# Performance work log

Hardware: AMD Instinct MI355X
Metric: run time of the kernel (lower is better)

Reference implementation:

```python
import jax, jax.numpy as jnp
import numpy as np
import math

GAMMA = 0.97      # discounting
LAM = 0.95        # gae lambda
EPSILON = 0.3     # ppo clip
EPS = 0.2         # gpo clip (eps)
ENT_COST = 0.01
RSCALE = 1.0
ALPHA = 1.0
NUM_STEPS = 1.0e6 # normalization step count buffer


def _mlp(x, Ws, bs):
    for i, (W, b) in enumerate(zip(Ws, bs)):
        x = x @ W.T + b
        if i < len(Ws) - 1:
            x = jax.nn.silu(x)
    return x


def _dist_create(logits):
    loc, s = jnp.split(logits, 2, axis=-1)
    return loc, jax.nn.softplus(s) + 0.001


def _log_det_jac(x):
    # tanh bijector log|det J| per element
    return 2.0 * (math.log(2.0) - x - jax.nn.softplus(-2.0 * x))


def _log_prob(loc, scale, dist):
    lu = -0.5 * jnp.square((dist - loc) / scale)
    ln = 0.5 * math.log(2.0 * math.pi) + jnp.log(scale)
    return (lu - ln - _log_det_jac(dist)).sum(-1)


def _entropy(loc, scale, noise):
    ln = 0.5 * math.log(2.0 * math.pi) + jnp.log(scale)
    ent = (0.5 + ln) * jnp.ones_like(loc)
    dist = loc + scale * noise  # reparameterized sample (torch.normal)
    return (ent + _log_det_jac(dist)).sum(-1)


def _kl(pl, ps, ql, qs):
    vr = jnp.square(ps / qs)
    t1 = jnp.square((pl - ql) / qs)
    return (0.5 * (vr + t1 - 1.0 - jnp.log(vr))).mean(-1)


def _normalize(obs, rm, rv):
    var = jnp.clip(rv / (NUM_STEPS + 1.0), 1e-6, 1e6)
    return jnp.clip((obs - rm) / jnp.sqrt(var), -5.0, 5.0)


def _gae(truncation, termination, reward, values, bootstrap_value):
    tm = 1.0 - truncation
    v1 = jnp.concatenate([values[1:], bootstrap_value[None]], 0)
    deltas = (reward + GAMMA * (1.0 - termination) * v1 - values) * tm

    def step(acc, xs):
        d, te, tmask = xs
        acc = d + GAMMA * (1.0 - te) * tmask * LAM * acc
        return acc, acc

    _, vmx = jax.lax.scan(step, jnp.zeros_like(bootstrap_value),
                          (deltas, termination, tm), reverse=True)
    vs = vmx + values
    vs1 = jnp.concatenate([vs[1:], bootstrap_value[None]], 0)
    adv = (reward + GAMMA * (1.0 - termination) * vs1 - values) * tm
    return vs, adv


def _loss(observation, pobservation, reward, done, truncation, logits, action,
          noise, pw0, pb0, pw1, pb1, pw2, pb2, vw0, vb0, vw1, vb1, vw2, vb2,
          running_mean, running_variance, kl_coef):
    sg = jax.lax.stop_gradient
    Pw, Pb = [pw0, pw1, pw2], [pb0, pb1, pb2]
    Vw, Vb = [vw0, vw1, vw2], [vb0, vb1, vb2]

    obs_n = _normalize(observation, running_mean, running_variance)
    pobs_n = _normalize(pobservation, running_mean, running_variance)

    guider_logits = _mlp(obs_n[:-1], Pw, Pb)
    learner_logits = _mlp(pobs_n[:-1], Pw, Pb)
    baseline = _mlp(obs_n, Vw, Vb).squeeze(-1)  # [T+1, B]
    bootstrap = baseline[-1]
    baseline = baseline[:-1]

    reward_s = reward * RSCALE
    termination = done * (1.0 - truncation)

    loc, scale = _dist_create(logits)
    b_lp = _log_prob(loc, scale, action)
    gl, gs = _dist_create(guider_logits)
    g_lp = _log_prob(gl, gs, action)
    ll, ls = _dist_create(learner_logits)
    l_lp = _log_prob(ll, ls, action)

    kl_learner = _kl(sg(gl), sg(gs), ll, ls).mean()
    kl_guider = _kl(gl, gs, sg(ll), sg(ls))
    # use_clip = True branch
    diff = g_lp - l_lp
    m = jnp.where(diff > math.log(1.0 + EPS), 1.0,
                  jnp.where(diff < math.log(1.0 - EPS), 1.0, 0.0))
    kl_guider = (kl_guider * m).mean()

    vs, adv = _gae(truncation, termination, reward_s, sg(baseline), sg(bootstrap))
    vs = sg(vs)
    adv = sg((adv - adv.mean()) / (jnp.std(adv, ddof=1) + 1e-5))

    rho = jnp.exp(g_lp - b_lp)
    rho_clip = jnp.exp(jnp.clip(g_lp - sg(l_lp), math.log(1.0 - EPS), math.log(1.0 + EPS))
                       + sg(l_lp) - b_lp)
    rho_clip = jnp.clip(rho_clip, 1.0 - EPSILON, 1.0 + EPSILON)
    guider_policy_loss = -jnp.mean(jnp.minimum(rho * adv, rho_clip * adv))

    rho2 = jnp.exp(jnp.minimum(l_lp - b_lp, 10.0))  # stable_exp
    rho2c = jnp.clip(rho2, 1.0 - EPSILON, 1.0 + EPSILON)
    learner_policy_loss = -jnp.mean(jnp.minimum(rho2 * adv, rho2c * adv))

    v_err = vs - baseline
    v_loss = jnp.mean(v_err * v_err) * 0.25

    entropy = jnp.mean(_entropy(loc, scale, noise))
    entropy_loss = -ENT_COST * entropy

    learner_loss = kl_learner + learner_policy_loss * ALPHA  # use_clip
    guider_loss = kl_guider + guider_policy_loss
    total = learner_loss + guider_loss + v_loss + entropy_loss
    return total, guider_loss, learner_loss, kl_learner


def setup_inputs() -> dict:
    key = jax.random.key(0)
    T, B, OBS, ACT, H = 1024, 256, 64, 8, 256
    ks = iter(jax.random.split(key, 32))

    def lin(fin, fout):
        W = jax.random.normal(next(ks), (fout, fin), jnp.float32) / np.float32(np.sqrt(fin))
        b = jnp.zeros((fout,), jnp.float32)
        return W, b

    pw0, pb0 = lin(OBS, H); pw1, pb1 = lin(H, H); pw2, pb2 = lin(H, 2 * ACT)
    vw0, vb0 = lin(OBS, H); vw1, vb1 = lin(H, H); vw2, vb2 = lin(H, 1)

    observation = jax.random.normal(next(ks), (T + 1, B, OBS), jnp.float32)
    pobservation = observation + 0.1 * jax.random.normal(next(ks), (T + 1, B, OBS), jnp.float32)
    reward = jax.random.normal(next(ks), (T, B), jnp.float32)
    done = (jax.random.uniform(next(ks), (T, B)) < 0.01).astype(jnp.float32)
    truncation = (jax.random.uniform(next(ks), (T, B)) < 0.005).astype(jnp.float32)
    logits = 0.5 * jax.random.normal(next(ks), (T, B, 2 * ACT), jnp.float32)
    action = jax.random.normal(next(ks), (T, B, ACT), jnp.float32)
    noise = jax.random.normal(next(ks), (T, B, ACT), jnp.float32)
    running_mean = jnp.zeros((OBS,), jnp.float32)
    running_variance = jnp.ones((OBS,), jnp.float32) * NUM_STEPS  # unit variance after /num_steps
    kl_coef = jnp.ones((1,), jnp.float32)

    return {"observation": observation, "pobservation": pobservation,
            "reward": reward, "done": done, "truncation": truncation,
            "logits": logits, "action": action, "noise": noise,
            "pw0": pw0, "pb0": pb0, "pw1": pw1, "pb1": pb1, "pw2": pw2, "pb2": pb2,
            "vw0": vw0, "vb0": vb0, "vw1": vw1, "vb1": vb1, "vw2": vw2, "vb2": vb2,
            "running_mean": running_mean, "running_variance": running_variance,
            "kl_coef": kl_coef}


def reference(observation, pobservation, reward, done, truncation, logits, action,
              noise, pw0, pb0, pw1, pb1, pw2, pb2, vw0, vb0, vw1, vb1, vw2, vb2,
              running_mean, running_variance, kl_coef):
    return _loss(observation, pobservation, reward, done, truncation, logits,
                 action, noise, pw0, pb0, pw1, pb1, pw2, pb2, vw0, vb0, vw1, vb1,
                 vw2, vb2, running_mean, running_variance, kl_coef)
```

## Files before the change

### kernel.cpp

```cpp
#include <hip/hip_runtime.h>
#include <math.h>

#define GAMMA_   0.97f
#define LAM_     0.95f
#define EPSILON_ 0.3f
#define HLOG2PI_ 0.91893853320467274f
#define LOG2C_   0.69314718055994531f
#define LOG1P2_  0.18232155679395463f
#define LOG0P8_  (-0.22314355131420976f)

typedef unsigned short u16;
typedef unsigned int   u32;
typedef _Float16 half8 __attribute__((ext_vector_type(8)));
typedef _Float16 half4 __attribute__((ext_vector_type(4)));
typedef __attribute__((ext_vector_type(4))) float floatx4;
typedef __attribute__((ext_vector_type(8))) float floatx8;

constexpr int  TT     = 1024;
constexpr long ROWS_P = (long)TT * 256;
constexpr long ROWS_V = (long)(TT + 1) * 256;

constexpr long FR_W0P_HI = 0;
constexpr long FR_W0P_LO = 16384;
constexpr long FR_W1P_HI = 32768;
constexpr long FR_W1P_LO = 98304;
constexpr long FR_W2P_HI = 163840;
constexpr long FR_W2P_LO = 167936;
constexpr long FR_W0V_HI = 172032;
constexpr long FR_W0V_LO = 188416;
constexpr long FR_W1V_HI = 204800;
constexpr long FR_W1V_LO = 270336;
constexpr long FR_W2V_HI = 335872;
constexpr long FR_W2V_LO = 339968;
constexpr long FR_TOTAL  = 344064;

constexpr long WS_ACC  = 0;
constexpr long WS_INV  = 32;
constexpr long WS_ADV  = 96;
constexpr long WS_BASE = WS_ADV + ROWS_P;
constexpr long WS_GA   = WS_BASE + ROWS_V;
constexpr long WS_GP   = WS_GA + 8192;
constexpr long WS_BANK = WS_GP + 8192;
constexpr long WS_GLP  = WS_BANK + 1024;
constexpr long WS_LLP  = WS_GLP + ROWS_P;
constexpr long WS_BLP  = WS_LLP + ROWS_P;


__device__ __forceinline__ float softplus_f(float x) {
  return (x > 20.f) ? x : log1pf(expf(x));
}
__device__ __forceinline__ float silu_f(float x) {
  return x * __builtin_amdgcn_rcpf(1.f + __expf(-x));
}
__device__ __forceinline__ float clamp30(float x) {
  return fminf(1e30f, fmaxf(-1e30f, x));
}

__global__ void convert_kernel(const float* __restrict__ pw0,
                               const float* __restrict__ pw1,
                               const float* __restrict__ pw2,
                               const float* __restrict__ vw0,
                               const float* __restrict__ vw1,
                               const float* __restrict__ vw2,
                               const float* __restrict__ rv,
                               float* __restrict__ inv_std,
                               float* __restrict__ accum,
                               float* __restrict__ accumB,
                               u16* __restrict__ frag) {
  if (blockIdx.x == 0) {
    int t = threadIdx.x;
    if (t < 32) accum[t] = 0.f;
    for (int i = t; i < 1024; i += 256) accumB[i] = 0.f;
    if (t < 64) {
      float var = rv[t] / 1000001.0f;
      var = fminf(1e6f, fmaxf(1e-6f, var));
      inv_std[t] = 1.f / sqrtf(var);
    }
  }
  int idx = blockIdx.x * 256 + threadIdx.x;
  const float* W; int kslog, K, nvalid; long hioff, looff; int e;
  if (idx < 16384)       { W = pw0; e = idx;          kslog = 1; K = 64;  nvalid = 256; hioff = FR_W0P_HI; looff = FR_W0P_LO; }
  else if (idx < 81920)  { W = pw1; e = idx - 16384;  kslog = 3; K = 256; nvalid = 256; hioff = FR_W1P_HI; looff = FR_W1P_LO; }
  else if (idx < 86016)  { W = pw2; e = idx - 81920;  kslog = 3; K = 256; nvalid = 16;  hioff = FR_W2P_HI; looff = FR_W2P_LO; }
  else if (idx < 102400) { W = vw0; e = idx - 86016;  kslog = 1; K = 64;  nvalid = 256; hioff = FR_W0V_HI; looff = FR_W0V_LO; }
  else if (idx < 167936) { W = vw1; e = idx - 102400; kslog = 3; K = 256; nvalid = 256; hioff = FR_W1V_HI; looff = FR_W1V_LO; }
  else                   { W = vw2; e = idx - 167936; kslog = 3; K = 256; nvalid = 1;   hioff = FR_W2V_HI; looff = FR_W2V_LO; }
  int j    = e & 7;
  int lane = (e >> 3) & 63;
  int ks   = (e >> 9) & ((1 << kslog) - 1);
  int nt   = e >> (9 + kslog);
  int n = nt * 16 + (lane & 15);
  int k = ks * 32 + ((lane >> 4) << 3) + j;
  float w = (n < nvalid) ? W[n * K + k] : 0.f;
  _Float16 hi = (_Float16)w;
  _Float16 lo = (_Float16)(w - (float)hi);
  frag[hioff + e] = *(u16*)&hi;
  frag[looff + e] = *(u16*)&lo;
}

constexpr int SX = 72;
constexpr int SH = 264;
constexpr int SO = 20;

__global__ __launch_bounds__(256, 3)
void fused_fwd_kernel(const float* __restrict__ obs,
                      const float* __restrict__ pobs,
                      const float* __restrict__ rm,
                      const float* __restrict__ inv_std,
                      const u16* __restrict__ frag,
                      const float* __restrict__ pb0,
                      const float* __restrict__ pb1,
                      const float* __restrict__ pb2,
                      const float* __restrict__ vb0,
                      const float* __restrict__ vb1,
                      const float* __restrict__ vb2,
                      const float* __restrict__ logits,
                      const float* __restrict__ action,
                      const float* __restrict__ noise,
                      float* __restrict__ baseline,
                      float* __restrict__ glpA,
                      float* __restrict__ llpA,
                      float* __restrict__ blpA,
                      float* __restrict__ accumB) {
  __shared__ __align__(16) _Float16 H[64 * SH];
  __shared__ __align__(16) float OUTT[64 * SO];
  __shared__ float red[192];

  const int tid  = threadIdx.x;
  const int lane = tid & 63;
  const int wv   = tid >> 6;
  const int lm   = lane & 15;
  const int lq   = lane >> 4;

  int bid = blockIdx.x;
  bool isP; long sub;
  if (bid < 12288) {
    int g = bid / 3, r = bid - g * 3;
    if (r < 2) { isP = true;  sub = (long)g * 2 + r; }
    else       { isP = false; sub = g; }
  } else { isP = false; sub = 4096 + (bid - 12288); }

  _Float16* X = H;

  if (isP) {
    const long row0 = sub * 32;
    #pragma unroll
    for (int it = 0; it < 2; ++it) {
      int flat = it * 256 + tid;
      int vr = flat >> 3;
      int f0 = (flat & 7) * 8;
      const float* src = (vr < 32) ? obs : pobs;
      floatx8 v  = *(const floatx8*)&src[(row0 + (vr & 31)) * 64 + f0];
      floatx8 m  = *(const floatx8*)&rm[f0];
      floatx8 is = *(const floatx8*)&inv_std[f0];
      half8 h;
      #pragma unroll
      for (int j = 0; j < 8; ++j)
        h[j] = (_Float16)fminf(5.f, fmaxf(-5.f, (v[j] - m[j]) * is[j]));
      *(half8*)&X[vr * SX + f0] = h;
    }

    const int  er   = tid >> 3;
    const int  ed   = tid & 7;
    const long erow = row0 + er;
    float pf_a   = action[erow * 8 + ed];
    float pf_loc = logits[erow * 16 + ed];
    float pf_sr  = logits[erow * 16 + 8 + ed];
    float pf_nd  = noise[erow * 8 + ed];

    const half8* B0h = (const half8*)(frag + FR_W0P_HI);
    const half8* B0l = (const half8*)(frag + FR_W0P_LO);
    half8 B0hr[2][4], B0lr[2][4];
    #pragma unroll
    for (int ks = 0; ks < 2; ++ks)
      #pragma unroll
      for (int nt = 0; nt < 4; ++nt) {
        int ntg = wv * 4 + nt;
        B0hr[ks][nt] = B0h[(ntg * 2 + ks) * 64 + lane];
        B0lr[ks][nt] = B0l[(ntg * 2 + ks) * 64 + lane];
      }

    floatx4 acc[4][4];
    #pragma unroll
    for (int nt = 0; nt < 4; ++nt) {
      floatx4 bz = *(const floatx4*)&pb0[(wv * 4 + nt) * 16 + lq * 4];
      #pragma unroll
      for (int mt = 0; mt < 4; ++mt) acc[mt][nt] = bz;
    }
    __syncthreads();

    #pragma unroll
    for (int ks = 0; ks < 2; ++ks) {
      half8 A[4];
      #pragma unroll
      for (int mt = 0; mt < 4; ++mt)
        A[mt] = *(const half8*)&X[(mt * 16 + lm) * SX + ks * 32 + lq * 8];
      __builtin_amdgcn_s_setprio(1);
      #pragma unroll
      for (int mt = 0; mt < 4; ++mt)
        #pragma unroll
        for (int nt = 0; nt < 4; ++nt)
          acc[mt][nt] = __builtin_amdgcn_mfma_f32_16x16x32_f16(B0hr[ks][nt], A[mt], acc[mt][nt], 0, 0, 0);
      #pragma unroll
      for (int mt = 0; mt < 4; ++mt)
        #pragma unroll
        for (int nt = 0; nt < 4; ++nt)
          acc[mt][nt] = __builtin_amdgcn_mfma_f32_16x16x32_f16(B0lr[ks][nt], A[mt], acc[mt][nt], 0, 0, 0);
      __builtin_amdgcn_s_setprio(0);
    }

    const half8* B1h = (const half8*)(frag + FR_W1P_HI);
    const half8* B1l = (const half8*)(frag + FR_W1P_LO);
    half8 Bh[4], Bl[4], Bhn[4], Bln[4];
    #pragma unroll
    for (int nt = 0; nt < 4; ++nt) {
      int ntg = wv * 4 + nt;
      Bh[nt] = B1h[(ntg * 8) * 64 + lane];
      Bl[nt] = B1l[(ntg * 8) * 64 + lane];
    }

    __syncthreads();
    #pragma unroll
    for (int nt = 0; nt < 4; ++nt) {
      int colbase = (wv * 4 + nt) * 16 + lq * 4;
      #pragma unroll
      for (int mt = 0; mt < 4; ++mt) {
        int row = mt * 16 + lm;
        half4 h;
        #pragma unroll
        for (int reg = 0; reg < 4; ++reg)
          h[reg] = (_Float16)silu_f(acc[mt][nt][reg]);
        *(half4*)&H[row * SH + colbase] = h;
      }
    }
    #pragma unroll
    for (int nt = 0; nt < 4; ++nt) {
      floatx4 bz = *(const floatx4*)&pb1[(wv * 4 + nt) * 16 + lq * 4];
      #pragma unroll
      for (int mt = 0; mt < 4; ++mt) acc[mt][nt] = bz;
    }
    __syncthreads();

    #pragma unroll 1
    for (int ks = 0; ks < 8; ++ks) {
      if (ks < 7) {
        #pragma unroll
        for (int nt = 0; nt < 4; ++nt) {
          int ntg = wv * 4 + nt;
          Bhn[nt] = B1h[(ntg * 8 + ks + 1) * 64 + lane];
          Bln[nt] = B1l[(ntg * 8 + ks + 1) * 64 + lane];
        }
      }
      half8 A[4];
      #pragma unroll
      for (int mt = 0; mt < 4; ++mt)
        A[mt] = *(const half8*)&H[(mt * 16 + lm) * SH + ks * 32 + lq * 8];
      __builtin_amdgcn_s_setprio(1);
      #pragma unroll
      for (int mt = 0; mt < 4; ++mt)
        #pragma unroll
        for (int nt = 0; nt < 4; ++nt)
          acc[mt][nt] = __builtin_amdgcn_mfma_f32_16x16x32_f16(Bh[nt], A[mt], acc[mt][nt], 0, 0, 0);
      #pragma unroll
      for (int mt = 0; mt < 4; ++mt)
        #pragma unroll
        for (int nt = 0; nt < 4; ++nt)
          acc[mt][nt] = __builtin_amdgcn_mfma_f32_16x16x32_f16(Bl[nt], A[mt], acc[mt][nt], 0, 0, 0);
      __builtin_amdgcn_s_setprio(0);
      if (ks < 7) {
        #pragma unroll
        for (int nt = 0; nt < 4; ++nt) { Bh[nt] = Bhn[nt]; Bl[nt] = Bln[nt]; }
      }
    }

    const half8* B2h = (const half8*)(frag + FR_W2P_HI);
    const half8* B2l = (const half8*)(frag + FR_W2P_LO);
    half8 B2hr[8], B2lr[8];
    #pragma unroll
    for (int ks = 0; ks < 8; ++ks) {
      B2hr[ks] = B2h[ks * 64 + lane];
      B2lr[ks] = B2l[ks * 64 + lane];
    }

    __syncthreads();
    #pragma unroll
    for (int nt = 0; nt < 4; ++nt) {
      int colbase = (wv * 4 + nt) * 16 + lq * 4;
      #pragma unroll
      for (int mt = 0; mt < 4; ++mt) {
        int row = mt * 16 + lm;
        half4 h;
        #pragma unroll
        for (int reg = 0; reg < 4; ++reg)
          h[reg] = (_Float16)silu_f(acc[mt][nt][reg]);
        *(half4*)&H[row * SH + colbase] = h;
      }
    }
    __syncthreads();

    {
      floatx4 c3a = (floatx4){0.f,0.f,0.f,0.f};
      floatx4 c3b = (floatx4){0.f,0.f,0.f,0.f};
      __builtin_amdgcn_s_setprio(1);
      #pragma unroll
      for (int ks = 0; ks < 8; ks += 2) {
        half8 A0 = *(const half8*)&H[(wv * 16 + lm) * SH + ks * 32 + lq * 8];
        half8 A1 = *(const half8*)&H[(wv * 16 + lm) * SH + (ks + 1) * 32 + lq * 8];
        c3a = __builtin_amdgcn_mfma_f32_16x16x32_f16(B2hr[ks],     A0, c3a, 0, 0, 0);
        c3b = __builtin_amdgcn_mfma_f32_16x16x32_f16(B2hr[ks + 1], A1, c3b, 0, 0, 0);
        c3a = __builtin_amdgcn_mfma_f32_16x16x32_f16(B2lr[ks],     A0, c3a, 0, 0, 0);
        c3b = __builtin_amdgcn_mfma_f32_16x16x32_f16(B2lr[ks + 1], A1, c3b, 0, 0, 0);
      }
      __builtin_amdgcn_s_setprio(0);
      floatx4 bias = *(const floatx4*)&pb2[lq * 4];
      floatx4 o = c3a + c3b + bias;
      #pragma unroll
      for (int reg = 0; reg < 4; ++reg)
        OUTT[(wv * 16 + lm) * SO + lq * 4 + reg] = o[reg];
    }
    __syncthreads();

    {
      int r = er, d = ed;
      float gl  = OUTT[r * SO + d];
      float gsr = OUTT[r * SO + 8 + d];
      float ll  = OUTT[(32 + r) * SO + d];
      float lsr = OUTT[(32 + r) * SO + 8 + d];
      float a   = pf_a;
      float loc = pf_loc;
      float sr  = pf_sr;
      float nd  = pf_nd;

      float gs = softplus_f(gsr) + 1e-3f;
      float ls = softplus_f(lsr) + 1e-3f;
      float sc = softplus_f(sr) + 1e-3f;
      float ldj = 2.f * (LOG2C_ - a - softplus_f(-2.f * a));
      float lgs = logf(gs), lls = logf(ls), lsc = logf(sc);
      float zg = (a - gl) / gs;
      float zl = (a - ll) / ls;
      float z  = (a - loc) / sc;
      float glp = -0.5f * zg * zg - lgs - HLOG2PI_ - ldj;
      float llp = -0.5f * zl * zl - lls - HLOG2PI_ - ldj;
      float blp = -0.5f * z * z - lsc - HLOG2PI_ - ldj;
      float ratio = gs / ls;
      float vr = ratio * ratio;
      float t1 = (gl - ll) / ls; t1 *= t1;
      float kl = 0.5f * (vr + t1 - 1.f) - (lgs - lls);
      float dist = loc + sc * nd;
      float ent = 0.5f + HLOG2PI_ + lsc
                + 2.f * (LOG2C_ - dist - softplus_f(-2.f * dist));

      #pragma unroll
      for (int o = 4; o > 0; o >>= 1) {
        glp += __shfl_down(glp, o, 8);
        llp += __shfl_down(llp, o, 8);
        blp += __shfl_down(blp, o, 8);
        kl  += __shfl_down(kl, o, 8);
        ent += __shfl_down(ent, o, 8);
      }

      if (d == 0) {
        kl *= 0.125f;
        kl  = clamp30(kl);
        ent = clamp30(ent);
        float diff = glp - llp;
        float m = (diff > LOG1P2_ || diff < LOG0P8_) ? 1.f : 0.f;
        red[r]        = kl;
        red[32 + r]   = kl * m;
        red[64 + r]   = ent;
        red[96 + r]   = glp;
        red[128 + r]  = llp;
        red[160 + r]  = blp;
      }
    }
    __syncthreads();
    if (tid < 96) {
      int a = tid >> 5, i = tid & 31;
      float v = red[96 + tid];
      float* dst = (a == 0) ? glpA : (a == 1) ? llpA : blpA;
      dst[row0 + i] = v;
    }
    if (tid < 32) {
      float s0 = red[tid], s1 = red[32 + tid], s2 = red[64 + tid];
      #pragma unroll
      for (int o = 16; o > 0; o >>= 1) {
        s0 += __shfl_down(s0, o, 32);
        s1 += __shfl_down(s1, o, 32);
        s2 += __shfl_down(s2, o, 32);
      }
      if (tid == 0) {
        float* bank = accumB + (bid & 31) * 32;
        atomicAdd(&bank[0], s0);
        atomicAdd(&bank[1], s1);
        atomicAdd(&bank[2], s2);
      }
    }
  } else {
    const long row0 = sub * 64;
    #pragma unroll
    for (int it = 0; it < 2; ++it) {
      int flat = it * 256 + tid;
      int vr = flat >> 3;
      int f0 = (flat & 7) * 8;
      floatx8 v  = *(const floatx8*)&obs[(row0 + vr) * 64 + f0];
      floatx8 m  = *(const floatx8*)&rm[f0];
      floatx8 is = *(const floatx8*)&inv_std[f0];
      half8 h;
      #pragma unroll
      for (int j = 0; j < 8; ++j)
        h[j] = (_Float16)fminf(5.f, fmaxf(-5.f, (v[j] - m[j]) * is[j]));
      *(half8*)&X[vr * SX + f0] = h;
    }

    const half8* B0h = (const half8*)(frag + FR_W0V_HI);
    const half8* B0l = (const half8*)(frag + FR_W0V_LO);
    half8 B0hr[2][4], B0lr[2][4];
    #pragma unroll
    for (int ks = 0; ks < 2; ++ks)
      #pragma unroll
      for (int nt = 0; nt < 4; ++nt) {
        int ntg = wv * 4 + nt;
        B0hr[ks][nt] = B0h[(ntg * 2 + ks) * 64 + lane];
        B0lr[ks][nt] = B0l[(ntg * 2 + ks) * 64 + lane];
      }

    floatx4 acc[4][4];
    #pragma unroll
    for (int nt = 0; nt < 4; ++nt) {
      floatx4 bz = *(const floatx4*)&vb0[(wv * 4 + nt) * 16 + lq * 4];
      #pragma unroll
      for (int mt = 0; mt < 4; ++mt) acc[mt][nt] = bz;
    }
    __syncthreads();

    #pragma unroll
    for (int ks = 0; ks < 2; ++ks) {
      half8 A[4];
      #pragma unroll
      for (int mt = 0; mt < 4; ++mt)
        A[mt] = *(const half8*)&X[(mt * 16 + lm) * SX + ks * 32 + lq * 8];
      __builtin_amdgcn_s_setprio(1);
      #pragma unroll
      for (int mt = 0; mt < 4; ++mt)
        #pragma unroll
        for (int nt = 0; nt < 4; ++nt)
          acc[mt][nt] = __builtin_amdgcn_mfma_f32_16x16x32_f16(B0hr[ks][nt], A[mt], acc[mt][nt], 0, 0, 0);
      #pragma unroll
      for (int mt = 0; mt < 4; ++mt)
        #pragma unroll
        for (int nt = 0; nt < 4; ++nt)
          acc[mt][nt] = __builtin_amdgcn_mfma_f32_16x16x32_f16(B0lr[ks][nt], A[mt], acc[mt][nt], 0, 0, 0);
      __builtin_amdgcn_s_setprio(0);
    }

    const half8* B1h = (const half8*)(frag + FR_W1V_HI);
    const half8* B1l = (const half8*)(frag + FR_W1V_LO);
    half8 Bh[4], Bl[4], Bhn[4], Bln[4];
    #pragma unroll
    for (int nt = 0; nt < 4; ++nt) {
      int ntg = wv * 4 + nt;
      Bh[nt] = B1h[(ntg * 8) * 64 + lane];
      Bl[nt] = B1l[(ntg * 8) * 64 + lane];
    }

    __syncthreads();
    #pragma unroll
    for (int nt = 0; nt < 4; ++nt) {
      int colbase = (wv * 4 + nt) * 16 + lq * 4;
      #pragma unroll
      for (int mt = 0; mt < 4; ++mt) {
        int row = mt * 16 + lm;
        half4 h;
        #pragma unroll
        for (int reg = 0; reg < 4; ++reg)
          h[reg] = (_Float16)silu_f(acc[mt][nt][reg]);
        *(half4*)&H[row * SH + colbase] = h;
      }
    }
    #pragma unroll
    for (int nt = 0; nt < 4; ++nt) {
      floatx4 bz = *(const floatx4*)&vb1[(wv * 4 + nt) * 16 + lq * 4];
      #pragma unroll
      for (int mt = 0; mt < 4; ++mt) acc[mt][nt] = bz;
    }
    __syncthreads();

    #pragma unroll 1
    for (int ks = 0; ks < 8; ++ks) {
      if (ks < 7) {
        #pragma unroll
        for (int nt = 0; nt < 4; ++nt) {
          int ntg = wv * 4 + nt;
          Bhn[nt] = B1h[(ntg * 8 + ks + 1) * 64 + lane];
          Bln[nt] = B1l[(ntg * 8 + ks + 1) * 64 + lane];
        }
      }
      half8 A[4];
      #pragma unroll
      for (int mt = 0; mt < 4; ++mt)
        A[mt] = *(const half8*)&H[(mt * 16 + lm) * SH + ks * 32 + lq * 8];
      __builtin_amdgcn_s_setprio(1);
      #pragma unroll
      for (int mt = 0; mt < 4; ++mt)
        #pragma unroll
        for (int nt = 0; nt < 4; ++nt)
          acc[mt][nt] = __builtin_amdgcn_mfma_f32_16x16x32_f16(Bh[nt], A[mt], acc[mt][nt], 0, 0, 0);
      #pragma unroll
      for (int mt = 0; mt < 4; ++mt)
        #pragma unroll
        for (int nt = 0; nt < 4; ++nt)
          acc[mt][nt] = __builtin_amdgcn_mfma_f32_16x16x32_f16(Bl[nt], A[mt], acc[mt][nt], 0, 0, 0);
      __builtin_amdgcn_s_setprio(0);
      if (ks < 7) {
        #pragma unroll
        for (int nt = 0; nt < 4; ++nt) { Bh[nt] = Bhn[nt]; Bl[nt] = Bln[nt]; }
      }
    }

    const half8* B2h = (const half8*)(frag + FR_W2V_HI);
    const half8* B2l = (const half8*)(frag + FR_W2V_LO);
    half8 B2hr[8], B2lr[8];
    #pragma unroll
    for (int ks = 0; ks < 8; ++ks) {
      B2hr[ks] = B2h[ks * 64 + lane];
      B2lr[ks] = B2l[ks * 64 + lane];
    }

    __syncthreads();
    #pragma unroll
    for (int nt = 0; nt < 4; ++nt) {
      int colbase = (wv * 4 + nt) * 16 + lq * 4;
      #pragma unroll
      for (int mt = 0; mt < 4; ++mt) {
        int row = mt * 16 + lm;
        half4 h;
        #pragma unroll
        for (int reg = 0; reg < 4; ++reg)
          h[reg] = (_Float16)silu_f(acc[mt][nt][reg]);
        *(half4*)&H[row * SH + colbase] = h;
      }
    }
    __syncthreads();

    {
      floatx4 c3a = (floatx4){0.f,0.f,0.f,0.f};
      floatx4 c3b = (floatx4){0.f,0.f,0.f,0.f};
      __builtin_amdgcn_s_setprio(1);
      #pragma unroll
      for (int ks = 0; ks < 8; ks += 2) {
        half8 A0 = *(const half8*)&H[(wv * 16 + lm) * SH + ks * 32 + lq * 8];
        half8 A1 = *(const half8*)&H[(wv * 16 + lm) * SH + (ks + 1) * 32 + lq * 8];
        c3a = __builtin_amdgcn_mfma_f32_16x16x32_f16(B2hr[ks],     A0, c3a, 0, 0, 0);
        c3b = __builtin_amdgcn_mfma_f32_16x16x32_f16(B2hr[ks + 1], A1, c3b, 0, 0, 0);
        c3a = __builtin_amdgcn_mfma_f32_16x16x32_f16(B2lr[ks],     A0, c3a, 0, 0, 0);
        c3b = __builtin_amdgcn_mfma_f32_16x16x32_f16(B2lr[ks + 1], A1, c3b, 0, 0, 0);
      }
      __builtin_amdgcn_s_setprio(0);
      if (lq == 0) baseline[row0 + wv * 16 + lm] = c3a[0] + c3b[0] + vb2[0];
    }
  }
}

__global__ void gae_phase1(const float* __restrict__ reward,
                           const float* __restrict__ done,
                           const float* __restrict__ trunc,
                           const float* __restrict__ baseline,
                           float* __restrict__ A, float* __restrict__ P) {
  int s = blockIdx.x, b = threadIdx.x;
  float Aa = 0.f, Pp = 1.f;
  for (int t = (s + 1) * 32 - 1; t >= s * 32; --t) {
    int idx = t * 256 + b;
    float r = reward[idx], d = done[idx], tr = trunc[idx];
    float tm = 1.f - tr;
    float te = d * tm;
    float bl = baseline[idx], bl1 = baseline[idx + 256];
    float g1 = GAMMA_ * (1.f - te);
    float delta = (r + g1 * bl1 - bl) * tm;
    float c = g1 * tm * LAM_;
    Aa = delta + c * Aa;
    Pp = c * Pp;
  }
  A[s * 256 + b] = Aa;
  P[s * 256 + b] = Pp;
}

__global__ void gae_phase3(const float* __restrict__ reward,
                           const float* __restrict__ done,
                           const float* __restrict__ trunc,
                           const float* __restrict__ baseline,
                           const float* __restrict__ A,
                           const float* __restrict__ P,
                           float* __restrict__ adv,
                           float* __restrict__ accum) {
  __shared__ float red[12];
  int s = blockIdx.x, b = threadIdx.x;
  float acc = 0.f;
  #pragma unroll 1
  for (int s2 = 31; s2 > s; --s2)
    acc = A[s2 * 256 + b] + P[s2 * 256 + b] * acc;
  int tend = (s + 1) * 32;
  float vnext = baseline[tend * 256 + b];
  float vs_next = acc + vnext;
  float sa = 0.f, sa2 = 0.f, sv2 = 0.f;
  for (int t = tend - 1; t >= s * 32; --t) {
    int idx = t * 256 + b;
    float r = reward[idx], d = done[idx], tr = trunc[idx];
    float tm = 1.f - tr;
    float te = d * tm;
    float bl = baseline[idx];
    float g1 = GAMMA_ * (1.f - te);
    float delta = (r + g1 * vnext - bl) * tm;
    acc = delta + g1 * tm * LAM_ * acc;
    float at = (r + g1 * vs_next - bl) * tm;
    at = fminf(1e15f, fmaxf(-1e15f, at));
    adv[idx] = at;
    sa += at; sa2 += at * at;
    sv2 += fminf(acc * acc, 1e30f);
    vs_next = acc + bl;
    vnext = bl;
  }
  float v0 = sa, v1 = sa2, v2 = sv2;
  #pragma unroll
  for (int o = 32; o > 0; o >>= 1) {
    v0 += __shfl_down(v0, o, 64);
    v1 += __shfl_down(v1, o, 64);
    v2 += __shfl_down(v2, o, 64);
  }
  int lane = threadIdx.x & 63, w = threadIdx.x >> 6;
  if (lane == 0) { red[w] = v0; red[4 + w] = v1; red[8 + w] = v2; }
  __syncthreads();
  if (threadIdx.x == 0) {
    float s0=0.f, s1=0.f, s2=0.f;
    for (int q = 0; q < 4; ++q) { s0 += red[q]; s1 += red[4+q]; s2 += red[8+q]; }
    atomicAdd(&accum[3], s0);
    atomicAdd(&accum[4], s1);
    atomicAdd(&accum[5], s2);
  }
}

__global__ __launch_bounds__(256)
void epi2_kernel(const float* __restrict__ glpA,
                 const float* __restrict__ llpA,
                 const float* __restrict__ blpA,
                 const float* __restrict__ adv,
                 float* __restrict__ accum,
                 float* __restrict__ accumB,
                 float* __restrict__ out) {
  __shared__ float red2[8];
  __shared__ int lastFlag;
  int tid = threadIdx.x;
  long row = (long)blockIdx.x * 256 + tid;

  float glp = glpA[row], llp = llpA[row], blp = blpA[row], av = adv[row];
  float N = (float)ROWS_P;
  float sum = accum[3], sumsq = accum[4];
  float mean = sum / N;
  float var  = fmaxf((sumsq - sum * sum / N) / (N - 1.f), 0.f);
  float inv  = 1.f / (sqrtf(var) + 1e-5f);
  float a_n  = (av - mean) * inv;

  float diff = glp - llp;
  float rho = expf(fminf(glp - blp, 80.f));
  float cl  = fminf(LOG1P2_, fmaxf(LOG0P8_, diff));
  float rc  = expf(fminf(cl + llp - blp, 80.f));
  rc = fminf(1.f + EPSILON_, fmaxf(1.f - EPSILON_, rc));
  float gp = clamp30(fminf(rho * a_n, rc * a_n));

  float rho2 = expf(fminf(llp - blp, 10.f));
  float r2c  = fminf(1.f + EPSILON_, fmaxf(1.f - EPSILON_, rho2));
  float lp = clamp30(fminf(rho2 * a_n, r2c * a_n));

  #pragma unroll
  for (int o = 32; o > 0; o >>= 1) {
    gp += __shfl_down(gp, o, 64);
    lp += __shfl_down(lp, o, 64);
  }
  int lane = tid & 63, w = tid >> 6;
  if (lane == 0) { red2[w] = gp; red2[4 + w] = lp; }
  __syncthreads();
  if (tid == 0) {
    float sg = 0.f, sl = 0.f;
    for (int q = 0; q < 4; ++q) { sg += red2[q]; sl += red2[4 + q]; }
    float* bank = accumB + (blockIdx.x & 31) * 32;
    atomicAdd(&bank[6], sg);
    atomicAdd(&bank[7], sl);
    __threadfence();
    u32 old = atomicAdd((u32*)&accum[24], 1u);
    lastFlag = (old == (u32)(gridDim.x - 1)) ? 1 : 0;
  }
  __syncthreads();
  if (lastFlag) {
    float s0 = 0.f, s1 = 0.f, s2 = 0.f, s6 = 0.f, s7 = 0.f;
    if (tid < 32) {
      float* bank = accumB + tid * 32;
      s0 = atomicAdd(&bank[0], 0.f);
      s1 = atomicAdd(&bank[1], 0.f);
      s2 = atomicAdd(&bank[2], 0.f);
      s6 = atomicAdd(&bank[6], 0.f);
      s7 = atomicAdd(&bank[7], 0.f);
    }
    #pragma unroll
    for (int o = 16; o > 0; o >>= 1) {
      s0 += __shfl_down(s0, o, 32);
      s1 += __shfl_down(s1, o, 32);
      s2 += __shfl_down(s2, o, 32);
      s6 += __shfl_down(s6, o, 32);
      s7 += __shfl_down(s7, o, 32);
    }
    if (tid == 0) {
      float kl_learner = s0 / N;
      float kl_guider  = s1 / N;
      float entropy    = s2 / N;
      float v_loss     = 0.25f * accum[5] / N;
      float gp_loss    = -s6 / N;
      float lp_loss    = -s7 / N;
      float learner_loss = kl_learner + lp_loss;
      float guider_loss  = kl_guider + gp_loss;
      float total = learner_loss + guider_loss + v_loss - 0.01f * entropy;
      out[0] = total;
      out[1] = guider_loss;
      out[2] = learner_loss;
      out[3] = kl_learner;
    }
  }
}

extern "C" void kernel_launch(void* const* d_in, const int* in_sizes, int n_in,
                              void* d_out, int out_size, void* d_ws, size_t ws_size,
                              hipStream_t stream) {
  (void)in_sizes; (void)n_in; (void)out_size; (void)ws_size;
  const float* obs    = (const float*)d_in[0];
  const float* pobs   = (const float*)d_in[1];
  const float* reward = (const float*)d_in[2];
  const float* done   = (const float*)d_in[3];
  const float* trunc  = (const float*)d_in[4];
  const float* logits = (const float*)d_in[5];
  const float* action = (const float*)d_in[6];
  const float* noise  = (const float*)d_in[7];
  const float* pw0 = (const float*)d_in[8];
  const float* pb0 = (const float*)d_in[9];
  const float* pw1 = (const float*)d_in[10];
  const float* pb1 = (const float*)d_in[11];
  const float* pw2 = (const float*)d_in[12];
  const float* pb2 = (const float*)d_in[13];
  const float* vw0 = (const float*)d_in[14];
  const float* vb0 = (const float*)d_in[15];
  const float* vw1 = (const float*)d_in[16];
  const float* vb1 = (const float*)d_in[17];
  const float* vw2 = (const float*)d_in[18];
  const float* vb2 = (const float*)d_in[19];
  const float* rm  = (const float*)d_in[20];
  const float* rv  = (const float*)d_in[21];

  u16*   frag  = (u16*)d_ws;
  float* fbase = (float*)d_ws + FR_TOTAL / 2;
  float* accum   = fbase + WS_ACC;
  float* inv_std = fbase + WS_INV;
  float* adv     = fbase + WS_ADV;
  float* base    = fbase + WS_BASE;
  float* gA      = fbase + WS_GA;
  float* gP      = fbase + WS_GP;
  float* accumB  = fbase + WS_BANK;
  float* glpA    = fbase + WS_GLP;
  float* llpA    = fbase + WS_LLP;
  float* blpA    = fbase + WS_BLP;
  float* out = (float*)d_out;

  convert_kernel<<<672, 256, 0, stream>>>(pw0, pw1, pw2, vw0, vw1, vw2,
                                          rv, inv_std, accum, accumB, frag);

  fused_fwd_kernel<<<12292, 256, 0, stream>>>(
      obs, pobs, rm, inv_std, frag, pb0, pb1, pb2, vb0, vb1, vb2,
      logits, action, noise, base, glpA, llpA, blpA, accumB);

  gae_phase1<<<32, 256, 0, stream>>>(reward, done, trunc, base, gA, gP);
  gae_phase3<<<32, 256, 0, stream>>>(reward, done, trunc, base, gA, gP,
                                     adv, accum);

  epi2_kernel<<<1024, 256, 0, stream>>>(glpA, llpA, blpA, adv,
                                        accum, accumB, out);
}
```

Before: 523.9 us.

## Merge GAE phases and epilogue into one cooperative kernel with grid syncs

Replaces three separate kernel launches (GAE phase 1, GAE phase 3 and the loss epilogue) with a single cooperative kernel of 256 blocks that uses grid.sync between stages. The epilogue now has each block handle four rows per thread, and the last-block atomic counter is replaced by a final grid sync after which block 0 reduces the banks. This aims to remove launch gaps and the ticket-based completion logic. In exchange the GAE stages run on only 32 of the 256 blocks while the rest wait at the barriers, and the kernel depends on cooperative launch support and co-residency of all blocks.

After: 598.4 us. 14.2% more time.

```diff
diff --git a/kernel.cpp b/kernel.cpp
--- a/kernel.cpp
+++ b/kernel.cpp
@@ -1,5 +1,8 @@
 #include <hip/hip_runtime.h>
+#include <hip/hip_cooperative_groups.h>
 #include <math.h>
+
+namespace cg = cooperative_groups;
 
 #define GAMMA_   0.97f
 #define LAM_     0.95f
@@ -561,143 +564,140 @@
   }
 }
 
-__global__ void gae_phase1(const float* __restrict__ reward,
-                           const float* __restrict__ done,
-                           const float* __restrict__ trunc,
-                           const float* __restrict__ baseline,
-                           float* __restrict__ A, float* __restrict__ P) {
-  int s = blockIdx.x, b = threadIdx.x;
-  float Aa = 0.f, Pp = 1.f;
-  for (int t = (s + 1) * 32 - 1; t >= s * 32; --t) {
-    int idx = t * 256 + b;
-    float r = reward[idx], d = done[idx], tr = trunc[idx];
-    float tm = 1.f - tr;
-    float te = d * tm;
-    float bl = baseline[idx], bl1 = baseline[idx + 256];
-    float g1 = GAMMA_ * (1.f - te);
-    float delta = (r + g1 * bl1 - bl) * tm;
-    float c = g1 * tm * LAM_;
-    Aa = delta + c * Aa;
-    Pp = c * Pp;
+__global__ __launch_bounds__(256)
+void gae_epi_kernel(const float* __restrict__ reward,
+                    const float* __restrict__ done,
+                    const float* __restrict__ trunc,
+                    const float* __restrict__ baseline,
+                    float* __restrict__ A, float* __restrict__ P,
+                    float* __restrict__ adv,
+                    const float* __restrict__ glpA,
+                    const float* __restrict__ llpA,
+                    const float* __restrict__ blpA,
+                    float* __restrict__ accum,
+                    float* __restrict__ accumB,
+                    float* __restrict__ out) {
+  cg::grid_group grid = cg::this_grid();
+  __shared__ float red[12];
+  __shared__ float red2[8];
+  const int tid = threadIdx.x;
+  const int bid = blockIdx.x;
+
+  if (bid < 32) {
+    int s = bid, b = tid;
+    float Aa = 0.f, Pp = 1.f;
+    for (int t = (s + 1) * 32 - 1; t >= s * 32; --t) {
+      int idx = t * 256 + b;
+      float r = reward[idx], d = done[idx], tr = trunc[idx];
+      float tm = 1.f - tr;
+      float te = d * tm;
+      float bl = baseline[idx], bl1 = baseline[idx + 256];
+      float g1 = GAMMA_ * (1.f - te);
+      float delta = (r + g1 * bl1 - bl) * tm;
+      float c = g1 * tm * LAM_;
+      Aa = delta + c * Aa;
+      Pp = c * Pp;
+    }
+    A[s * 256 + b] = Aa;
+    P[s * 256 + b] = Pp;
   }
-  A[s * 256 + b] = Aa;
-  P[s * 256 + b] = Pp;
-}
-
-__global__ void gae_phase3(const float* __restrict__ reward,
-                           const float* __restrict__ done,
-                           const float* __restrict__ trunc,
-                           const float* __restrict__ baseline,
-                           const float* __restrict__ A,
-                           const float* __restrict__ P,
-                           float* __restrict__ adv,
-                           float* __restrict__ accum) {
-  __shared__ float red[12];
-  int s = blockIdx.x, b = threadIdx.x;
-  float acc = 0.f;
-  #pragma unroll 1
-  for (int s2 = 31; s2 > s; --s2)
-    acc = A[s2 * 256 + b] + P[s2 * 256 + b] * acc;
-  int tend = (s + 1) * 32;
-  float vnext = baseline[tend * 256 + b];
-  float vs_next = acc + vnext;
-  float sa = 0.f, sa2 = 0.f, sv2 = 0.f;
-  for (int t = tend - 1; t >= s * 32; --t) {
-    int idx = t * 256 + b;
-    float r = reward[idx], d = done[idx], tr = trunc[idx];
-    float tm = 1.f - tr;
-    float te = d * tm;
-    float bl = baseline[idx];
-    float g1 = GAMMA_ * (1.f - te);
-    float delta = (r + g1 * vnext - bl) * tm;
-    acc = delta + g1 * tm * LAM_ * acc;
-    float at = (r + g1 * vs_next - bl) * tm;
-    at = fminf(1e15f, fmaxf(-1e15f, at));
-    adv[idx] = at;
-    sa += at; sa2 += at * at;
-    sv2 += fminf(acc * acc, 1e30f);
-    vs_next = acc + bl;
-    vnext = bl;
+  grid.sync();
+
+  if (bid < 32) {
+    int s = bid, b = tid;
+    float acc = 0.f;
+    #pragma unroll 1
+    for (int s2 = 31; s2 > s; --s2)
+      acc = A[s2 * 256 + b] + P[s2 * 256 + b] * acc;
+    int tend = (s + 1) * 32;
+    float vnext = baseline[tend * 256 + b];
+    float vs_next = acc + vnext;
+    float sa = 0.f, sa2 = 0.f, sv2 = 0.f;
+    for (int t = tend - 1; t >= s * 32; --t) {
+      int idx = t * 256 + b;
+      float r = reward[idx], d = done[idx], tr = trunc[idx];
+      float tm = 1.f - tr;
+      float te = d * tm;
+      float bl = baseline[idx];
+      float g1 = GAMMA_ * (1.f - te);
+      float delta = (r + g1 * vnext - bl) * tm;
+      acc = delta + g1 * tm * LAM_ * acc;
+      float at = (r + g1 * vs_next - bl) * tm;
+      at = fminf(1e15f, fmaxf(-1e15f, at));
+      adv[idx] = at;
+      sa += at; sa2 += at * at;
+      sv2 += fminf(acc * acc, 1e30f);
+      vs_next = acc + bl;
+      vnext = bl;
+    }
+    float v0 = sa, v1 = sa2, v2 = sv2;
+    #pragma unroll
+    for (int o = 32; o > 0; o >>= 1) {
+      v0 += __shfl_down(v0, o, 64);
+      v1 += __shfl_down(v1, o, 64);
+      v2 += __shfl_down(v2, o, 64);
+    }
+    int lane = tid & 63, w = tid >> 6;
+    if (lane == 0) { red[w] = v0; red[4 + w] = v1; red[8 + w] = v2; }
+    __syncthreads();
+    if (tid == 0) {
+      float s0 = 0.f, s1 = 0.f, s2 = 0.f;
+      for (int q = 0; q < 4; ++q) { s0 += red[q]; s1 += red[4+q]; s2 += red[8+q]; }
+      atomicAdd(&accum[3], s0);
+      atomicAdd(&accum[4], s1);
+      atomicAdd(&accum[5], s2);
+    }
   }
-  float v0 = sa, v1 = sa2, v2 = sv2;
-  #pragma unroll
-  for (int o = 32; o > 0; o >>= 1) {
-    v0 += __shfl_down(v0, o, 64);
-    v1 += __shfl_down(v1, o, 64);
-    v2 += __shfl_down(v2, o, 64);
+  grid.sync();
+
+  {
+    float N = (float)ROWS_P;
+    float sum = accum[3], sumsq = accum[4];
+    float mean = sum / N;
+    float var  = fmaxf((sumsq - sum * sum / N) / (N - 1.f), 0.f);
+    float inv  = 1.f / (sqrtf(var) + 1e-5f);
+
+    float gpT = 0.f, lpT = 0.f;
+    #pragma unroll
+    for (int i = 0; i < 4; ++i) {
+      long row = (long)i * 65536 + (long)bid * 256 + tid;
+      float glp = glpA[row], llp = llpA[row], blp = blpA[row];
+      float a_n = (adv[row] - mean) * inv;
+
+      float diff = glp - llp;
+      float rho = expf(fminf(glp - blp, 80.f));
+      float cl  = fminf(LOG1P2_, fmaxf(LOG0P8_, diff));
+      float rc  = expf(fminf(cl + llp - blp, 80.f));
+      rc = fminf(1.f + EPSILON_, fmaxf(1.f - EPSILON_, rc));
+      gpT += clamp30(fminf(rho * a_n, rc * a_n));
+
+      float rho2 = expf(fminf(llp - blp, 10.f));
+      float r2c  = fminf(1.f + EPSILON_, fmaxf(1.f - EPSILON_, rho2));
+      lpT += clamp30(fminf(rho2 * a_n, r2c * a_n));
+    }
+    #pragma unroll
+    for (int o = 32; o > 0; o >>= 1) {
+      gpT += __shfl_down(gpT, o, 64);
+      lpT += __shfl_down(lpT, o, 64);
+    }
+    int lane = tid & 63, w = tid >> 6;
+    if (lane == 0) { red2[w] = gpT; red2[4 + w] = lpT; }
+    __syncthreads();
+    if (tid == 0) {
+      float sg = 0.f, sl = 0.f;
+      for (int q = 0; q < 4; ++q) { sg += red2[q]; sl += red2[4 + q]; }
+      float* bank = accumB + (bid & 31) * 32;
+      atomicAdd(&bank[6], sg);
+      atomicAdd(&bank[7], sl);
+    }
   }
-  int lane = threadIdx.x & 63, w = threadIdx.x >> 6;
-  if (lane == 0) { red[w] = v0; red[4 + w] = v1; red[8 + w] = v2; }
-  __syncthreads();
-  if (threadIdx.x == 0) {
-    float s0=0.f, s1=0.f, s2=0.f;
-    for (int q = 0; q < 4; ++q) { s0 += red[q]; s1 += red[4+q]; s2 += red[8+q]; }
-    atomicAdd(&accum[3], s0);
-    atomicAdd(&accum[4], s1);
-    atomicAdd(&accum[5], s2);
-  }
-}
-
-__global__ __launch_bounds__(256)
-void epi2_kernel(const float* __restrict__ glpA,
-                 const float* __restrict__ llpA,
-                 const float* __restrict__ blpA,
-                 const float* __restrict__ adv,
-                 float* __restrict__ accum,
-                 float* __restrict__ accumB,
-                 float* __restrict__ out) {
-  __shared__ float red2[8];
-  __shared__ int lastFlag;
-  int tid = threadIdx.x;
-  long row = (long)blockIdx.x * 256 + tid;
-
-  float glp = glpA[row], llp = llpA[row], blp = blpA[row], av = adv[row];
-  float N = (float)ROWS_P;
-  float sum = accum[3], sumsq = accum[4];
-  float mean = sum / N;
-  float var  = fmaxf((sumsq - sum * sum / N) / (N - 1.f), 0.f);
-  float inv  = 1.f / (sqrtf(var) + 1e-5f);
-  float a_n  = (av - mean) * inv;
-
-  float diff = glp - llp;
-  float rho = expf(fminf(glp - blp, 80.f));
-  float cl  = fminf(LOG1P2_, fmaxf(LOG0P8_, diff));
-  float rc  = expf(fminf(cl + llp - blp, 80.f));
-  rc = fminf(1.f + EPSILON_, fmaxf(1.f - EPSILON_, rc));
-  float gp = clamp30(fminf(rho * a_n, rc * a_n));
-
-  float rho2 = expf(fminf(llp - blp, 10.f));
-  float r2c  = fminf(1.f + EPSILON_, fmaxf(1.f - EPSILON_, rho2));
-  float lp = clamp30(fminf(rho2 * a_n, r2c * a_n));
-
-  #pragma unroll
-  for (int o = 32; o > 0; o >>= 1) {
-    gp += __shfl_down(gp, o, 64);
-    lp += __shfl_down(lp, o, 64);
-  }
-  int lane = tid & 63, w = tid >> 6;
-  if (lane == 0) { red2[w] = gp; red2[4 + w] = lp; }
-  __syncthreads();
-  if (tid == 0) {
-    float sg = 0.f, sl = 0.f;
-    for (int q = 0; q < 4; ++q) { sg += red2[q]; sl += red2[4 + q]; }
-    float* bank = accumB + (blockIdx.x & 31) * 32;
-    atomicAdd(&bank[6], sg);
-    atomicAdd(&bank[7], sl);
-    __threadfence();
-    u32 old = atomicAdd((u32*)&accum[24], 1u);
-    lastFlag = (old == (u32)(gridDim.x - 1)) ? 1 : 0;
-  }
-  __syncthreads();
-  if (lastFlag) {
+  grid.sync();
+
+  if (bid == 0) {
     float s0 = 0.f, s1 = 0.f, s2 = 0.f, s6 = 0.f, s7 = 0.f;
     if (tid < 32) {
-      float* bank = accumB + tid * 32;
-      s0 = atomicAdd(&bank[0], 0.f);
-      s1 = atomicAdd(&bank[1], 0.f);
-      s2 = atomicAdd(&bank[2], 0.f);
-      s6 = atomicAdd(&bank[6], 0.f);
-      s7 = atomicAdd(&bank[7], 0.f);
+      const float* bank = accumB + tid * 32;
+      s0 = bank[0]; s1 = bank[1]; s2 = bank[2]; s6 = bank[6]; s7 = bank[7];
     }
     #pragma unroll
     for (int o = 16; o > 0; o >>= 1) {
@@ -708,6 +708,7 @@
       s7 += __shfl_down(s7, o, 32);
     }
     if (tid == 0) {
+      float N = (float)ROWS_P;
       float kl_learner = s0 / N;
       float kl_guider  = s1 / N;
       float entropy    = s2 / N;
@@ -773,10 +774,14 @@
       obs, pobs, rm, inv_std, frag, pb0, pb1, pb2, vb0, vb1, vb2,
       logits, action, noise, base, glpA, llpA, blpA, accumB);
 
-  gae_phase1<<<32, 256, 0, stream>>>(reward, done, trunc, base, gA, gP);
-  gae_phase3<<<32, 256, 0, stream>>>(reward, done, trunc, base, gA, gP,
-                                     adv, accum);
-
-  epi2_kernel<<<1024, 256, 0, stream>>>(glpA, llpA, blpA, adv,
-                                        accum, accumB, out);
+  {
+    void* args[] = {
+      (void*)&reward, (void*)&done, (void*)&trunc, (void*)&base,
+      (void*)&gA, (void*)&gP, (void*)&adv,
+      (void*)&glpA, (void*)&llpA, (void*)&blpA,
+      (void*)&accum, (void*)&accumB, (void*)&out
+    };
+    hipLaunchCooperativeKernel((void*)gae_epi_kernel, dim3(256), dim3(256),
+                               args, 0, stream);
+  }
 }
```
